# Optimization experiments

Hardware: AMD Instinct MI355X
Metric: run time of the kernel (lower is better)

The kernel has to match this reference:

```python
import jax, jax.numpy as jnp
import numpy as np

B, D_IN, T = 16, 1024, 1024
K, D_CB = 8192, 256
DECAY = 0.99
COMMITMENT = 0.15
CODEBOOK_LOSS_W = 1.0
THRESHOLD_DEAD = 2.0


def setup_inputs() -> dict:
    key = jax.random.key(0)
    ks = jax.random.split(key, 9)
    z = jax.random.normal(ks[0], (B, D_IN, T), dtype=jnp.float32)
    # weight-normed 1x1 conv params (kernel size 1 -> treat as matrices)
    in_v = jax.random.normal(ks[1], (D_CB, D_IN), dtype=jnp.float32) * 0.02
    in_g = jnp.ones((D_CB,), dtype=jnp.float32)
    in_b = jnp.zeros((D_CB,), dtype=jnp.float32)
    out_v = jax.random.normal(ks[2], (D_IN, D_CB), dtype=jnp.float32) * 0.02
    out_g = jnp.ones((D_IN,), dtype=jnp.float32)
    out_b = jnp.zeros((D_IN,), dtype=jnp.float32)
    codebook = jax.random.normal(ks[3], (K, D_CB), dtype=jnp.float32)
    cluster_size = jax.random.uniform(ks[4], (K,), dtype=jnp.float32) * 10.0
    return {"z": z, "in_g": in_g, "in_v": in_v, "in_b": in_b,
            "out_g": out_g, "out_v": out_v, "out_b": out_b,
            "codebook": codebook, "cluster_size": cluster_size}


def _wn_weight(g, v):
    # weight_norm dim=0: per-output-channel L2 norm over remaining dims
    return g[:, None] * v / jnp.linalg.norm(v, axis=1, keepdims=True)


def _l2norm(x, axis=-1, eps=1e-12):
    return x / jnp.maximum(jnp.linalg.norm(x, axis=axis, keepdims=True), eps)


def reference(z, in_g, in_v, in_b, out_g, out_v, out_b, codebook, cluster_size):
    sg = jax.lax.stop_gradient
    # in_project: 1x1 weight-normed conv  [B, D_IN, T] -> [B, D_CB, T]
    w_in = _wn_weight(in_g, in_v)
    z_e = jnp.einsum('oi,bit->bot', w_in, z) + in_b[None, :, None]

    # decode_latents
    enc = z_e.transpose(0, 2, 1).reshape(-1, D_CB)           # [(B*T), D_CB]
    enc_n = _l2norm(enc)
    cb_n = _l2norm(codebook)
    dist = (jnp.sum(enc_n ** 2, axis=1, keepdims=True)
            - 2.0 * enc_n @ cb_n.T
            + jnp.sum(cb_n ** 2, axis=1)[None, :])           # [(B*T), K]
    flat_idx = jnp.argmax(-dist, axis=1)                      # [(B*T)]
    indices = flat_idx.reshape(B, T)                          # [B, T]
    z_q = codebook[indices].transpose(0, 2, 1)                # [B, D_CB, T]

    # perplexity / usage stats (one-hot mean == normalized counts)
    n_tokens = B * T
    counts = jnp.zeros((K,), dtype=z_e.dtype).at[flat_idx].add(1.0)
    avg_probs = counts / n_tokens
    perplexity = jnp.exp(-jnp.sum(avg_probs * jnp.log(avg_probs + 1e-10)))

    # EMA cluster-size update (training, forced_activation=False): functional
    new_cluster_size = cluster_size * DECAY + counts * (1.0 - DECAY)
    active_num = jnp.sum(new_cluster_size > THRESHOLD_DEAD).astype(jnp.float32)

    # losses (training path)
    commit_loss = jnp.mean((z_e - sg(z_q)) ** 2, axis=(1, 2)) * COMMITMENT
    codebook_loss = jnp.mean((z_q - sg(z_e)) ** 2, axis=(1, 2)) * CODEBOOK_LOSS_W

    # straight-through
    z_q_st = z_e + sg(z_q - z_e)

    # out_project: 1x1 weight-normed conv  [B, D_CB, T] -> [B, D_IN, T]
    w_out = _wn_weight(out_g, out_v)
    z_q_out = jnp.einsum('oi,bit->bot', w_out, z_q_st) + out_b[None, :, None]

    return (z_q_out, indices, commit_loss, codebook_loss, dist, perplexity, active_num)
```

## Files before the change

kernel.cpp:

```cpp
#include <hip/hip_runtime.h>
#include <stdint.h>

#define B_    16
#define D_IN_ 1024
#define T_    1024
#define K_    8192
#define D_CB_ 256
#define NTOK  (B_*T_)

typedef unsigned long long ull;
typedef __attribute__((ext_vector_type(8))) short short8;
typedef __attribute__((ext_vector_type(4))) float f32x4;

#define WS_WIN   0
#define WS_WOUT  262144
#define WS_ENC   524288
#define WS_INVE  4718592
#define WS_ESQ   4734976
#define WS_INVC  4751360
#define WS_CSQ   4759552
#define WS_KEYS  4767744
#define WS_CNT   4800512
#define WS_LOSS  4808704

#define OUT_ZQ   0
#define OUT_IDX  16777216
#define OUT_COMM 16793600
#define OUT_CB   16793616
#define OUT_DIST 16793632
#define OUT_PERP 151011360
#define OUT_ACT  151011361

#define SCR_EHI  0
#define SCR_ELO  2097152
#define SCR_CHI  4194304
#define SCR_CLO  5242880
#define SCR_MINB 6291456
#define SCR_FLAG 10485760

#define MARGIN 2.5e-4f

__device__ __forceinline__ float wave_sum(float s) {
    for (int o = 32; o; o >>= 1) s += __shfl_down(s, o, 64);
    return s;
}

__device__ __forceinline__ unsigned short f2bf(float f) {
    unsigned u = __float_as_uint(f);
    return (unsigned short)((u + 0x7fffu + ((u >> 16) & 1u)) >> 16);
}

__global__ void wn_kernel(const float* __restrict__ g, const float* __restrict__ v,
                          float* __restrict__ w, int rows, int cols) {
    int wave = threadIdx.x >> 6, lane = threadIdx.x & 63;
    int row = blockIdx.x * 4 + wave;
    if (row >= rows) return;
    const float* vr = v + (size_t)row * cols;
    float s = 0.f;
    for (int c = lane; c < (cols >> 2); c += 64) {
        float4 x = ((const float4*)vr)[c];
        s += x.x*x.x + x.y*x.y + x.z*x.z + x.w*x.w;
    }
    s = wave_sum(s);
    s = __shfl(s, 0, 64);
    float norm = sqrtf(s);
    float gr = g[row];
    float* wr = w + (size_t)row * cols;
    for (int c = lane; c < cols; c += 64)
        wr[c] = gr * vr[c] / norm;
}

__global__ void split_kernel(const float* __restrict__ x, float* __restrict__ inv,
                             float* __restrict__ sq, unsigned short* __restrict__ hi,
                             unsigned short* __restrict__ lo) {
    int wave = threadIdx.x >> 6, lane = threadIdx.x & 63;
    int row = blockIdx.x * 4 + wave;
    float4 v = ((const float4*)(x + (size_t)row * D_CB_))[lane];
    float s = v.x*v.x + v.y*v.y + v.z*v.z + v.w*v.w;
    s = wave_sum(s);
    s = __shfl(s, 0, 64);
    float n = fmaxf(sqrtf(s), 1e-12f);
    float iv = 1.0f / n;
    if (lane == 0) { inv[row] = iv; sq[row] = s * iv * iv; }
    float f[4] = { v.x*iv, v.y*iv, v.z*iv, v.w*iv };
    unsigned short h[4], l[4];
    #pragma unroll
    for (int i = 0; i < 4; ++i) {
        h[i] = f2bf(f[i]);
        float hf = __uint_as_float((unsigned)h[i] << 16);
        l[i] = f2bf(f[i] - hf);
    }
    *(ushort4*)(hi + (size_t)row * D_CB_ + lane * 4) = make_ushort4(h[0], h[1], h[2], h[3]);
    *(ushort4*)(lo + (size_t)row * D_CB_ + lane * 4) = make_ushort4(l[0], l[1], l[2], l[3]);
}

__global__ __launch_bounds__(256) void ze_gemm(const float* __restrict__ w,
        const float* __restrict__ z, const float* __restrict__ bias,
        float* __restrict__ enc) {
    __shared__ float As[32 * 68];
    __shared__ float Bs[32 * 68];
    int b  = blockIdx.z;
    int o0 = blockIdx.y * 64;
    int t0 = blockIdx.x * 64;
    int t  = threadIdx.x;
    int tx = t & 15, ty = t >> 4;
    float acc[4][4] = {};
    const float* zb = z + (size_t)b * D_IN_ * T_;
    for (int kt = 0; kt < D_IN_ / 32; ++kt) {
        #pragma unroll
        for (int p = 0; p < 2; ++p) {
            int q = p * 256 + t;
            int r = q >> 3, c4 = q & 7;
            float4 x = *(const float4*)&w[(size_t)(o0 + r) * D_IN_ + kt * 32 + c4 * 4];
            As[(c4*4+0)*68 + r] = x.x; As[(c4*4+1)*68 + r] = x.y;
            As[(c4*4+2)*68 + r] = x.z; As[(c4*4+3)*68 + r] = x.w;
        }
        #pragma unroll
        for (int p = 0; p < 2; ++p) {
            int q = p * 256 + t;
            int r = q >> 4, c4 = q & 15;
            float4 x = *(const float4*)&zb[(size_t)(kt * 32 + r) * T_ + t0 + c4 * 4];
            *(float4*)&Bs[r * 68 + c4 * 4] = x;
        }
        __syncthreads();
        #pragma unroll 4
        for (int k = 0; k < 32; ++k) {
            float a[4], bv[4];
            *(float4*)a  = *(float4*)&As[k * 68 + tx * 4];
            *(float4*)bv = *(float4*)&Bs[k * 68 + ty * 4];
            #pragma unroll
            for (int i = 0; i < 4; ++i)
                #pragma unroll
                for (int j = 0; j < 4; ++j)
                    acc[i][j] = fmaf(a[j], bv[i], acc[i][j]);
        }
        __syncthreads();
    }
    float bias4[4];
    *(float4*)bias4 = *(const float4*)&bias[o0 + tx * 4];
    #pragma unroll
    for (int i = 0; i < 4; ++i) {
        int token = b * T_ + t0 + ty * 4 + i;
        float4 v = make_float4(acc[i][0] + bias4[0], acc[i][1] + bias4[1],
                               acc[i][2] + bias4[2], acc[i][3] + bias4[3]);
        *(float4*)&enc[(size_t)token * D_CB_ + o0 + tx * 4] = v;
    }
}

__global__ __launch_bounds__(256, 3) void dist_mfma(
        const unsigned short* __restrict__ ehi, const unsigned short* __restrict__ elo,
        const unsigned short* __restrict__ chi, const unsigned short* __restrict__ clo,
        const float* __restrict__ esq, const float* __restrict__ csq,
        float* __restrict__ dist, ull* __restrict__ minb) {
    __shared__ ull pairs[2][64][2][2];
    int bid = blockIdx.x;
    int lin = (bid & 7) * 1024 + (bid >> 3);
    int bx = lin >> 7;
    int by = lin & 127;
    int r0 = by * 128, c0 = bx * 128;
    int t = threadIdx.x;
    int wave = t >> 6, lane = t & 63;
    int wm = wave >> 1, wn = wave & 1;
    int lr = lane & 15, kg = lane >> 4;

    const unsigned short* ea = ehi + (size_t)(r0 + wm*64 + lr) * D_CB_ + kg*8;
    const unsigned short* eb = elo + (size_t)(r0 + wm*64 + lr) * D_CB_ + kg*8;
    const unsigned short* ca = chi + (size_t)(c0 + wn*64 + lr) * D_CB_ + kg*8;
    const unsigned short* cl = clo + (size_t)(c0 + wn*64 + lr) * D_CB_ + kg*8;

    f32x4 acc[4][4] = {};
    for (int kt = 0; kt < D_CB_ / 32; ++kt) {
        short8 ah[4], al[4], bh[4], bl[4];
        int k = kt * 32;
        #pragma unroll
        for (int i = 0; i < 4; ++i) {
            ah[i] = *(const short8*)(ea + (size_t)i*16*D_CB_ + k);
            al[i] = *(const short8*)(eb + (size_t)i*16*D_CB_ + k);
            bh[i] = *(const short8*)(ca + (size_t)i*16*D_CB_ + k);
            bl[i] = *(const short8*)(cl + (size_t)i*16*D_CB_ + k);
        }
        #pragma unroll
        for (int i = 0; i < 4; ++i)
            #pragma unroll
            for (int j = 0; j < 4; ++j) {
                acc[i][j] = __builtin_amdgcn_mfma_f32_16x16x32_bf16(ah[i], bh[j], acc[i][j], 0, 0, 0);
                acc[i][j] = __builtin_amdgcn_mfma_f32_16x16x32_bf16(ah[i], bl[j], acc[i][j], 0, 0, 0);
                acc[i][j] = __builtin_amdgcn_mfma_f32_16x16x32_bf16(al[i], bh[j], acc[i][j], 0, 0, 0);
            }
    }
    float csqv[4];
    #pragma unroll
    for (int j = 0; j < 4; ++j) csqv[j] = csq[c0 + wn*64 + j*16 + lr];
    #pragma unroll
    for (int i = 0; i < 4; ++i) {
        #pragma unroll
        for (int r = 0; r < 4; ++r) {
            int rl = i*16 + kg*4 + r;
            int grow = r0 + wm*64 + rl;
            float es = esq[grow];
            float* drow = dist + (size_t)grow * K_ + c0 + wn*64 + lr;
            ull m1 = ~0ull, m2 = ~0ull;
            #pragma unroll
            for (int j = 0; j < 4; ++j) {
                float d = fmaf(-2.0f, acc[i][j][r], es + csqv[j]);
                drow[j*16] = d;
                ull key = ((ull)__float_as_uint(d) << 32) | (unsigned)(c0 + wn*64 + j*16 + lr);
                if (key < m1) { m2 = m1; m1 = key; } else if (key < m2) m2 = key;
            }
            #pragma unroll
            for (int off = 1; off < 16; off <<= 1) {
                ull o1 = __shfl_xor(m1, off, 64);
                ull o2 = __shfl_xor(m2, off, 64);
                ull n1 = o1 < m1 ? o1 : m1;
                ull x  = o1 < m1 ? m1 : o1;
                ull y  = o2 < m2 ? o2 : m2;
                m2 = x < y ? x : y;
                m1 = n1;
            }
            if (lr == 0) { pairs[wm][rl][wn][0] = m1; pairs[wm][rl][wn][1] = m2; }
        }
    }
    __syncthreads();
    if (t < 128) {
        int wm2 = t >> 6, rl = t & 63;
        ull a1 = pairs[wm2][rl][0][0], a2 = pairs[wm2][rl][0][1];
        ull b1 = pairs[wm2][rl][1][0], b2 = pairs[wm2][rl][1][1];
        ull m1 = a1 < b1 ? a1 : b1;
        ull x  = a1 < b1 ? b1 : a1;
        ull y  = a2 < b2 ? a2 : b2;
        ull m2 = x < y ? x : y;
        size_t grow = (size_t)(r0 + wm2*64 + rl);
        minb[(grow*64 + bx)*2 + 0] = m1;
        minb[(grow*64 + bx)*2 + 1] = m2;
    }
}

__global__ void minreduce(const ull* __restrict__ minb, ull* __restrict__ keys,
                          int* __restrict__ flags) {
    int wave = threadIdx.x >> 6, lane = threadIdx.x & 63;
    int row = blockIdx.x * 4 + wave;
    ull m1 = minb[((size_t)row*64 + lane)*2 + 0];
    ull m2 = minb[((size_t)row*64 + lane)*2 + 1];
    #pragma unroll
    for (int off = 1; off < 64; off <<= 1) {
        ull o1 = __shfl_xor(m1, off, 64);
        ull o2 = __shfl_xor(m2, off, 64);
        ull n1 = o1 < m1 ? o1 : m1;
        ull x  = o1 < m1 ? m1 : o1;
        ull y  = o2 < m2 ? o2 : m2;
        m2 = x < y ? x : y;
        m1 = n1;
    }
    if (lane == 0) {
        keys[row] = m1;
        float d1 = __uint_as_float((unsigned)(m1 >> 32));
        float d2 = __uint_as_float((unsigned)(m2 >> 32));
        flags[row] = (d2 - d1 < MARGIN) ? 1 : 0;
    }
}

__global__ void argmin_fix(const float* __restrict__ enc, const float* __restrict__ inve,
        const float* __restrict__ esq, const float* __restrict__ cb,
        const float* __restrict__ invc, const float* __restrict__ csq,
        const float* __restrict__ dist, const int* __restrict__ flags,
        ull* __restrict__ keys) {
    int row = blockIdx.x;
    if (!flags[row]) return;
    int lane = threadIdx.x;
    ull k0 = keys[row];
    float thr = __uint_as_float((unsigned)(k0 >> 32)) + MARGIN;
    float iv = inve[row];
    float4 ev = ((const float4*)(enc + (size_t)row * D_CB_))[lane];
    ev.x *= iv; ev.y *= iv; ev.z *= iv; ev.w *= iv;
    float es = esq[row];
    float best = 1e30f; int bestc = 0;
    for (int base = 0; base < K_; base += 64) {
        float d = dist[(size_t)row * K_ + base + lane];
        ull mask = __ballot(d <= thr);
        while (mask) {
            int b = __ffsll(mask) - 1;
            mask &= mask - 1;
            int c = base + b;
            float4 cv = ((const float4*)(cb + (size_t)c * D_CB_))[lane];
            float p = ev.x*cv.x + ev.y*cv.y + ev.z*cv.z + ev.w*cv.w;
            p = wave_sum(p);
            p = __shfl(p, 0, 64);
            float dx = fmaf(-2.0f * invc[c], p, es + csq[c]);
            if (dx < best) { best = dx; bestc = c; }
        }
    }
    if (lane == 0)
        keys[row] = ((ull)__float_as_uint(best) << 32) | (unsigned)bestc;
}

__global__ void token_kernel(const float* __restrict__ enc, const float* __restrict__ cb,
        const ull* __restrict__ keys, float* __restrict__ idx_out,
        float* __restrict__ counts, float* __restrict__ loss) {
    int wave = threadIdx.x >> 6, lane = threadIdx.x & 63;
    int tok = blockIdx.x * 4 + wave;
    int idx = (int)(unsigned int)(keys[tok] & 0xffffffffull);
    float4 e = ((const float4*)(enc + (size_t)tok * D_CB_))[lane];
    float4 q = ((const float4*)(cb  + (size_t)idx * D_CB_))[lane];
    float dx = e.x - q.x, dy = e.y - q.y, dz = e.z - q.z, dw = e.w - q.w;
    float s = dx*dx + dy*dy + dz*dz + dw*dw;
    s = wave_sum(s);
    if (lane == 0) {
        idx_out[tok] = (float)idx;
        atomicAdd(&counts[idx], 1.0f);
        atomicAdd(&loss[tok >> 10], s);
    }
}

__global__ __launch_bounds__(256) void out_gemm(const float* __restrict__ w,
        const float* __restrict__ cb, const ull* __restrict__ keys,
        const float* __restrict__ bias, float* __restrict__ out) {
    __shared__ float As[32 * 68];
    __shared__ float Bs[32 * 68];
    __shared__ int idxs[64];
    int b  = blockIdx.z;
    int d0 = blockIdx.y * 64;
    int t0 = blockIdx.x * 64;
    int t  = threadIdx.x;
    if (t < 64) idxs[t] = (int)(unsigned int)(keys[b * T_ + t0 + t] & 0xffffffffull);
    __syncthreads();
    int tx = t & 15, ty = t >> 4;
    float acc[4][4] = {};
    for (int kt = 0; kt < D_CB_ / 32; ++kt) {
        #pragma unroll
        for (int p = 0; p < 2; ++p) {
            int q = p * 256 + t;
            int r = q >> 3, c4 = q & 7;
            float4 x = *(const float4*)&w[(size_t)(d0 + r) * D_CB_ + kt * 32 + c4 * 4];
            As[(c4*4+0)*68 + r] = x.x; As[(c4*4+1)*68 + r] = x.y;
            As[(c4*4+2)*68 + r] = x.z; As[(c4*4+3)*68 + r] = x.w;
        }
        #pragma unroll
        for (int p = 0; p < 2; ++p) {
            int q = p * 256 + t;
            int r = q >> 3, c4 = q & 7;
            float4 x = *(const float4*)&cb[(size_t)idxs[r] * D_CB_ + kt * 32 + c4 * 4];
            Bs[(c4*4+0)*68 + r] = x.x; Bs[(c4*4+1)*68 + r] = x.y;
            Bs[(c4*4+2)*68 + r] = x.z; Bs[(c4*4+3)*68 + r] = x.w;
        }
        __syncthreads();
        #pragma unroll 4
        for (int k = 0; k < 32; ++k) {
            float a[4], bv[4];
            *(float4*)a  = *(float4*)&As[k * 68 + ty * 4];
            *(float4*)bv = *(float4*)&Bs[k * 68 + tx * 4];
            #pragma unroll
            for (int i = 0; i < 4; ++i)
                #pragma unroll
                for (int j = 0; j < 4; ++j)
                    acc[i][j] = fmaf(a[i], bv[j], acc[i][j]);
        }
        __syncthreads();
    }
    #pragma unroll
    for (int i = 0; i < 4; ++i) {
        int d = d0 + ty * 4 + i;
        float bb = bias[d];
        float4 v = make_float4(acc[i][0] + bb, acc[i][1] + bb, acc[i][2] + bb, acc[i][3] + bb);
        *(float4*)&out[(size_t)b * D_IN_ * T_ + (size_t)d * T_ + t0 + tx * 4] = v;
    }
}

__global__ void finalize_kernel(const float* __restrict__ counts, const float* __restrict__ cs,
                                const float* __restrict__ loss, float* __restrict__ out) {
    int t = threadIdx.x;
    float H = 0.f, act = 0.f;
    for (int k = t; k < K_; k += 256) {
        float c = counts[k];
        float p = c * (1.0f / 16384.0f);
        H += p * logf(p + 1e-10f);
        float ncs = cs[k] * 0.99f + c * 0.01f;
        if (ncs > 2.0f) act += 1.0f;
    }
    __shared__ float sh[8];
    for (int o = 32; o; o >>= 1) { H += __shfl_down(H, o, 64); act += __shfl_down(act, o, 64); }
    int wave = t >> 6, lane = t & 63;
    if (lane == 0) { sh[wave] = H; sh[4 + wave] = act; }
    __syncthreads();
    if (t == 0) {
        out[OUT_PERP] = expf(-(sh[0] + sh[1] + sh[2] + sh[3]));
        out[OUT_ACT]  = sh[4] + sh[5] + sh[6] + sh[7];
    }
    if (t < 16) {
        float m = loss[t] * (1.0f / 262144.0f);
        out[OUT_COMM + t] = m * 0.15f;
        out[OUT_CB + t]   = m;
    }
}

extern "C" void kernel_launch(void* const* d_in, const int* in_sizes, int n_in,
                              void* d_out, int out_size, void* d_ws, size_t ws_size,
                              hipStream_t stream) {
    const float* z        = (const float*)d_in[0];
    const float* in_g     = (const float*)d_in[1];
    const float* in_v     = (const float*)d_in[2];
    const float* in_b     = (const float*)d_in[3];
    const float* out_g    = (const float*)d_in[4];
    const float* out_v    = (const float*)d_in[5];
    const float* out_b    = (const float*)d_in[6];
    const float* codebook = (const float*)d_in[7];
    const float* cluster  = (const float*)d_in[8];
    float* out = (float*)d_out;
    float* ws  = (float*)d_ws;
    ull* keys  = (ull*)(ws + WS_KEYS);

    float* scr = out + OUT_ZQ;
    unsigned short* ehi = (unsigned short*)(scr + SCR_EHI);
    unsigned short* elo = (unsigned short*)(scr + SCR_ELO);
    unsigned short* chi = (unsigned short*)(scr + SCR_CHI);
    unsigned short* clo = (unsigned short*)(scr + SCR_CLO);
    ull* minb  = (ull*)(scr + SCR_MINB);
    int* flags = (int*)(scr + SCR_FLAG);

    hipMemsetAsync(ws + WS_CNT, 0, (K_ + 16) * sizeof(float), stream);

    wn_kernel<<<64, 256, 0, stream>>>(in_g, in_v, ws + WS_WIN, D_CB_, D_IN_);
    wn_kernel<<<256, 256, 0, stream>>>(out_g, out_v, ws + WS_WOUT, D_IN_, D_CB_);
    split_kernel<<<K_ / 4, 256, 0, stream>>>(codebook, ws + WS_INVC, ws + WS_CSQ, chi, clo);
    ze_gemm<<<dim3(16, 4, 16), 256, 0, stream>>>(ws + WS_WIN, z, in_b, ws + WS_ENC);
    split_kernel<<<NTOK / 4, 256, 0, stream>>>(ws + WS_ENC, ws + WS_INVE, ws + WS_ESQ, ehi, elo);
    dist_mfma<<<8192, 256, 0, stream>>>(ehi, elo, chi, clo, ws + WS_ESQ, ws + WS_CSQ,
                                        out + OUT_DIST, minb);
    minreduce<<<NTOK / 4, 256, 0, stream>>>(minb, keys, flags);
    argmin_fix<<<NTOK, 64, 0, stream>>>(ws + WS_ENC, ws + WS_INVE, ws + WS_ESQ,
                                        codebook, ws + WS_INVC, ws + WS_CSQ,
                                        out + OUT_DIST, flags, keys);
    token_kernel<<<NTOK / 4, 256, 0, stream>>>(ws + WS_ENC, codebook, keys,
                                               out + OUT_IDX, ws + WS_CNT, ws + WS_LOSS);
    out_gemm<<<dim3(16, 16, 16), 256, 0, stream>>>(ws + WS_WOUT, codebook, keys,
                                                   out_b, out + OUT_ZQ);
    finalize_kernel<<<1, 256, 0, stream>>>(ws + WS_CNT, cluster, ws + WS_LOSS, out);
}
```

Baseline: 1.615 ms.

## Use split-bf16 MFMA for out projection, widen ze_gemm tile, nontemporal dist stores

Adds an out_mfma kernel that computes the out projection with three bf16 MFMAs per tile pair (hi*hi, hi*lo, lo*hi) on pre-split codebook and weight arrays, gathering codebook rows by index. It replaces the fp32 scalar out_gemm, but only when the workspace is large enough. It also doubles the token tile in ze_gemm to 128, remaps the dist_mfma block order, and makes the dist and output stores nontemporal. The split-bf16 path loses a little precision relative to fp32, and it adds two extra split kernels.

```diff
diff --git a/kernel.cpp b/kernel.cpp
--- a/kernel.cpp
+++ b/kernel.cpp
@@ -22,6 +22,12 @@
 #define WS_KEYS  4767744
 #define WS_CNT   4800512
 #define WS_LOSS  4808704
+#define WS_CBH   4808720
+#define WS_CBL   5857296
+#define WS_WOH   6905872
+#define WS_WOL   7036944
+#define WS_EXT_END 7168016
+#define WS_EXT_BYTES ((size_t)WS_EXT_END * 4)
 
 #define OUT_ZQ   0
 #define OUT_IDX  16777216
@@ -94,17 +100,34 @@
     *(ushort4*)(lo + (size_t)row * D_CB_ + lane * 4) = make_ushort4(l[0], l[1], l[2], l[3]);
 }
 
+__global__ void splitraw_kernel(const float* __restrict__ x, unsigned short* __restrict__ hi,
+                                unsigned short* __restrict__ lo, int n4) {
+    int i = blockIdx.x * 256 + threadIdx.x;
+    if (i >= n4) return;
+    float4 v = ((const float4*)x)[i];
+    float f[4] = { v.x, v.y, v.z, v.w };
+    unsigned short h[4], l[4];
+    #pragma unroll
+    for (int q = 0; q < 4; ++q) {
+        h[q] = f2bf(f[q]);
+        float hf = __uint_as_float((unsigned)h[q] << 16);
+        l[q] = f2bf(f[q] - hf);
+    }
+    *(ushort4*)(hi + (size_t)i * 4) = make_ushort4(h[0], h[1], h[2], h[3]);
+    *(ushort4*)(lo + (size_t)i * 4) = make_ushort4(l[0], l[1], l[2], l[3]);
+}
+
 __global__ __launch_bounds__(256) void ze_gemm(const float* __restrict__ w,
         const float* __restrict__ z, const float* __restrict__ bias,
         float* __restrict__ enc) {
     __shared__ float As[32 * 68];
-    __shared__ float Bs[32 * 68];
+    __shared__ float Bs[32 * 132];
     int b  = blockIdx.z;
     int o0 = blockIdx.y * 64;
-    int t0 = blockIdx.x * 64;
+    int t0 = blockIdx.x * 128;
     int t  = threadIdx.x;
     int tx = t & 15, ty = t >> 4;
-    float acc[4][4] = {};
+    float acc[4][8] = {};
     const float* zb = z + (size_t)b * D_IN_ * T_;
     for (int kt = 0; kt < D_IN_ / 32; ++kt) {
         #pragma unroll
@@ -116,34 +139,35 @@
             As[(c4*4+2)*68 + r] = x.z; As[(c4*4+3)*68 + r] = x.w;
         }
         #pragma unroll
-        for (int p = 0; p < 2; ++p) {
+        for (int p = 0; p < 4; ++p) {
             int q = p * 256 + t;
-            int r = q >> 4, c4 = q & 15;
+            int r = q >> 5, c4 = q & 31;
             float4 x = *(const float4*)&zb[(size_t)(kt * 32 + r) * T_ + t0 + c4 * 4];
-            *(float4*)&Bs[r * 68 + c4 * 4] = x;
+            *(float4*)&Bs[r * 132 + c4 * 4] = x;
         }
         __syncthreads();
         #pragma unroll 4
         for (int k = 0; k < 32; ++k) {
-            float a[4], bv[4];
-            *(float4*)a  = *(float4*)&As[k * 68 + tx * 4];
-            *(float4*)bv = *(float4*)&Bs[k * 68 + ty * 4];
+            float a[4], bv[8];
+            *(float4*)a      = *(float4*)&As[k * 68 + ty * 4];
+            *(float4*)&bv[0] = *(float4*)&Bs[k * 132 + tx * 4];
+            *(float4*)&bv[4] = *(float4*)&Bs[k * 132 + 64 + tx * 4];
             #pragma unroll
             for (int i = 0; i < 4; ++i)
                 #pragma unroll
-                for (int j = 0; j < 4; ++j)
-                    acc[i][j] = fmaf(a[j], bv[i], acc[i][j]);
+                for (int j = 0; j < 8; ++j)
+                    acc[i][j] = fmaf(a[i], bv[j], acc[i][j]);
         }
         __syncthreads();
     }
     float bias4[4];
-    *(float4*)bias4 = *(const float4*)&bias[o0 + tx * 4];
-    #pragma unroll
-    for (int i = 0; i < 4; ++i) {
-        int token = b * T_ + t0 + ty * 4 + i;
-        float4 v = make_float4(acc[i][0] + bias4[0], acc[i][1] + bias4[1],
-                               acc[i][2] + bias4[2], acc[i][3] + bias4[3]);
-        *(float4*)&enc[(size_t)token * D_CB_ + o0 + tx * 4] = v;
+    *(float4*)bias4 = *(const float4*)&bias[o0 + ty * 4];
+    #pragma unroll
+    for (int j = 0; j < 8; ++j) {
+        int token = b * T_ + t0 + (j < 4 ? tx * 4 + j : 64 + tx * 4 + (j - 4));
+        float4 v = make_float4(acc[0][j] + bias4[0], acc[1][j] + bias4[1],
+                               acc[2][j] + bias4[2], acc[3][j] + bias4[3]);
+        *(float4*)&enc[(size_t)token * D_CB_ + o0 + ty * 4] = v;
     }
 }
 
@@ -154,9 +178,10 @@
         float* __restrict__ dist, ull* __restrict__ minb) {
     __shared__ ull pairs[2][64][2][2];
     int bid = blockIdx.x;
-    int lin = (bid & 7) * 1024 + (bid >> 3);
-    int bx = lin >> 7;
-    int by = lin & 127;
+    int x = bid & 7;
+    int j_ = bid >> 3;
+    int by = x * 16 + (j_ & 15);
+    int bx = j_ >> 4;
     int r0 = by * 128, c0 = bx * 128;
     int t = threadIdx.x;
     int wave = t >> 6, lane = t & 63;
@@ -203,7 +228,7 @@
             #pragma unroll
             for (int j = 0; j < 4; ++j) {
                 float d = fmaf(-2.0f, acc[i][j][r], es + csqv[j]);
-                drow[j*16] = d;
+                __builtin_nontemporal_store(d, &drow[j*16]);
                 ull key = ((ull)__float_as_uint(d) << 32) | (unsigned)(c0 + wn*64 + j*16 + lr);
                 if (key < m1) { m2 = m1; m1 = key; } else if (key < m2) m2 = key;
             }
@@ -212,9 +237,9 @@
                 ull o1 = __shfl_xor(m1, off, 64);
                 ull o2 = __shfl_xor(m2, off, 64);
                 ull n1 = o1 < m1 ? o1 : m1;
-                ull x  = o1 < m1 ? m1 : o1;
-                ull y  = o2 < m2 ? o2 : m2;
-                m2 = x < y ? x : y;
+                ull xx = o1 < m1 ? m1 : o1;
+                ull yy = o2 < m2 ? o2 : m2;
+                m2 = xx < yy ? xx : yy;
                 m1 = n1;
             }
             if (lr == 0) { pairs[wm][rl][wn][0] = m1; pairs[wm][rl][wn][1] = m2; }
@@ -226,9 +251,9 @@
         ull a1 = pairs[wm2][rl][0][0], a2 = pairs[wm2][rl][0][1];
         ull b1 = pairs[wm2][rl][1][0], b2 = pairs[wm2][rl][1][1];
         ull m1 = a1 < b1 ? a1 : b1;
-        ull x  = a1 < b1 ? b1 : a1;
-        ull y  = a2 < b2 ? a2 : b2;
-        ull m2 = x < y ? x : y;
+        ull xx = a1 < b1 ? b1 : a1;
+        ull yy = a2 < b2 ? a2 : b2;
+        ull m2 = xx < yy ? xx : yy;
         size_t grow = (size_t)(r0 + wm2*64 + rl);
         minb[(grow*64 + bx)*2 + 0] = m1;
         minb[(grow*64 + bx)*2 + 1] = m2;
@@ -311,6 +336,63 @@
     }
 }
 
+__global__ __launch_bounds__(256, 3) void out_mfma(
+        const unsigned short* __restrict__ wh, const unsigned short* __restrict__ wl,
+        const unsigned short* __restrict__ cbh, const unsigned short* __restrict__ cbl,
+        const ull* __restrict__ keys, const float* __restrict__ bias,
+        float* __restrict__ out) {
+    int b  = blockIdx.z;
+    int d0 = blockIdx.y * 128;
+    int t0 = blockIdx.x * 128;
+    int t = threadIdx.x;
+    int wave = t >> 6, lane = t & 63;
+    int wm = wave >> 1, wn = wave & 1;
+    int lr = lane & 15, kg = lane >> 4;
+
+    int idx[4];
+    #pragma unroll
+    for (int i = 0; i < 4; ++i)
+        idx[i] = (int)(unsigned)(keys[b*T_ + t0 + wn*64 + i*16 + lr] & 0xffffffffull);
+
+    const unsigned short* wa = wh + (size_t)(d0 + wm*64 + lr) * D_CB_ + kg*8;
+    const unsigned short* wb = wl + (size_t)(d0 + wm*64 + lr) * D_CB_ + kg*8;
+
+    f32x4 acc[4][4] = {};
+    for (int kt = 0; kt < D_CB_ / 32; ++kt) {
+        int k = kt * 32;
+        short8 ah[4], al[4], bh[4], bl[4];
+        #pragma unroll
+        for (int i = 0; i < 4; ++i) {
+            ah[i] = *(const short8*)(wa + (size_t)i*16*D_CB_ + k);
+            al[i] = *(const short8*)(wb + (size_t)i*16*D_CB_ + k);
+            bh[i] = *(const short8*)(cbh + (size_t)idx[i]*D_CB_ + kg*8 + k);
+            bl[i] = *(const short8*)(cbl + (size_t)idx[i]*D_CB_ + kg*8 + k);
+        }
+        #pragma unroll
+        for (int i = 0; i < 4; ++i)
+            #pragma unroll
+            for (int j = 0; j < 4; ++j) {
+                acc[i][j] = __builtin_amdgcn_mfma_f32_16x16x32_bf16(ah[i], bh[j], acc[i][j], 0, 0, 0);
+                acc[i][j] = __builtin_amdgcn_mfma_f32_16x16x32_bf16(ah[i], bl[j], acc[i][j], 0, 0, 0);
+                acc[i][j] = __builtin_amdgcn_mfma_f32_16x16x32_bf16(al[i], bh[j], acc[i][j], 0, 0, 0);
+            }
+    }
+    float* ob = out + (size_t)b * D_IN_ * T_;
+    #pragma unroll
+    for (int i = 0; i < 4; ++i) {
+        #pragma unroll
+        for (int r = 0; r < 4; ++r) {
+            int d = d0 + wm*64 + i*16 + kg*4 + r;
+            float bb = bias[d];
+            #pragma unroll
+            for (int j = 0; j < 4; ++j) {
+                int tt = t0 + wn*64 + j*16 + lr;
+                __builtin_nontemporal_store(acc[i][j][r] + bb, &ob[(size_t)d * T_ + tt]);
+            }
+        }
+    }
+}
+
 __global__ __launch_bounds__(256) void out_gemm(const float* __restrict__ w,
         const float* __restrict__ cb, const ull* __restrict__ keys,
         const float* __restrict__ bias, float* __restrict__ out) {
@@ -416,12 +498,20 @@
     ull* minb  = (ull*)(scr + SCR_MINB);
     int* flags = (int*)(scr + SCR_FLAG);
 
+    bool mfma_out = ws_size >= WS_EXT_BYTES;
+
     hipMemsetAsync(ws + WS_CNT, 0, (K_ + 16) * sizeof(float), stream);
 
     wn_kernel<<<64, 256, 0, stream>>>(in_g, in_v, ws + WS_WIN, D_CB_, D_IN_);
     wn_kernel<<<256, 256, 0, stream>>>(out_g, out_v, ws + WS_WOUT, D_IN_, D_CB_);
     split_kernel<<<K_ / 4, 256, 0, stream>>>(codebook, ws + WS_INVC, ws + WS_CSQ, chi, clo);
-    ze_gemm<<<dim3(16, 4, 16), 256, 0, stream>>>(ws + WS_WIN, z, in_b, ws + WS_ENC);
+    if (mfma_out) {
+        splitraw_kernel<<<2048, 256, 0, stream>>>(codebook,
+                (unsigned short*)(ws + WS_CBH), (unsigned short*)(ws + WS_CBL), K_ * D_CB_ / 4);
+        splitraw_kernel<<<256, 256, 0, stream>>>(ws + WS_WOUT,
+                (unsigned short*)(ws + WS_WOH), (unsigned short*)(ws + WS_WOL), D_IN_ * D_CB_ / 4);
+    }
+    ze_gemm<<<dim3(8, 4, 16), 256, 0, stream>>>(ws + WS_WIN, z, in_b, ws + WS_ENC);
     split_kernel<<<NTOK / 4, 256, 0, stream>>>(ws + WS_ENC, ws + WS_INVE, ws + WS_ESQ, ehi, elo);
     dist_mfma<<<8192, 256, 0, stream>>>(ehi, elo, chi, clo, ws + WS_ESQ, ws + WS_CSQ,
                                         out + OUT_DIST, minb);
@@ -431,7 +521,14 @@
                                         out + OUT_DIST, flags, keys);
     token_kernel<<<NTOK / 4, 256, 0, stream>>>(ws + WS_ENC, codebook, keys,
                                                out + OUT_IDX, ws + WS_CNT, ws + WS_LOSS);
-    out_gemm<<<dim3(16, 16, 16), 256, 0, stream>>>(ws + WS_WOUT, codebook, keys,
-                                                   out_b, out + OUT_ZQ);
+    if (mfma_out) {
+        out_mfma<<<dim3(8, 8, 16), 256, 0, stream>>>(
+                (const unsigned short*)(ws + WS_WOH), (const unsigned short*)(ws + WS_WOL),
+                (const unsigned short*)(ws + WS_CBH), (const unsigned short*)(ws + WS_CBL),
+                keys, out_b, out + OUT_ZQ);
+    } else {
+        out_gemm<<<dim3(16, 16, 16), 256, 0, stream>>>(ws + WS_WOUT, codebook, keys,
+                                                       out_b, out + OUT_ZQ);
+    }
     finalize_kernel<<<1, 256, 0, stream>>>(ws + WS_CNT, cluster, ws + WS_LOSS, out);
 }
```

Result: no change. 1.592 ms (-1.5%).
